# Kernel optimization log

Hardware: AMD Instinct MI355X
Metric: run time of the kernel (lower is better)

The kernel has to match this reference:

```python
import jax, jax.numpy as jnp
import numpy as np

EMBED, HEADS, LEVELS, POINTS = 256, 8, 4, 4
SPATIAL_SHAPES = np.array([[128, 128], [64, 64], [32, 32], [16, 16]], dtype=np.int32)


def _grid_init_bias():
    # Faithful reproduction of the sampling_offsets bias init (per-head directional grid).
    thetas = np.arange(HEADS, dtype=np.float32) * (2.0 * np.pi / HEADS)
    g = np.stack([np.cos(thetas), np.sin(thetas)], -1)
    g = g / np.abs(g).max(-1, keepdims=True)
    g = np.tile(g.reshape(HEADS, 1, 1, 2), (1, LEVELS, POINTS, 1))
    for i in range(POINTS):
        g[:, :, i, :] *= i + 1
    return g.reshape(-1).astype(np.float32)


def setup_inputs() -> dict:
    key = jax.random.key(0)
    ks = jax.random.split(key, 8)
    bs = 2
    V = int((SPATIAL_SHAPES[:, 0] * SPATIAL_SHAPES[:, 1]).sum())  # 21760
    Q = V  # encoder self-attention
    C = EMBED
    n_off = HEADS * LEVELS * POINTS * 2
    n_attn = HEADS * LEVELS * POINTS
    inv_sqrt_c = 1.0 / np.sqrt(C)
    return {
        "query": jax.random.normal(ks[0], (bs, Q, C), jnp.float32),
        "value": jax.random.normal(ks[1], (bs, V, C), jnp.float32),
        "reference_points": jax.random.uniform(ks[2], (bs, Q, LEVELS, 2), jnp.float32),
        "spatial_shapes": SPATIAL_SHAPES,  # static int array
        # learned parameters (torch Linear stored as [in, out]: y = x @ W + b)
        "W_off": jax.random.normal(ks[3], (C, n_off), jnp.float32) * 0.01,
        "b_off": jnp.asarray(_grid_init_bias()),
        "W_attn": jax.random.normal(ks[4], (C, n_attn), jnp.float32) * 0.02,
        "b_attn": jnp.zeros((n_attn,), jnp.float32),
        "W_v": jax.random.normal(ks[5], (C, C), jnp.float32) * inv_sqrt_c,
        "b_v": jnp.zeros((C,), jnp.float32),
        "W_out": jax.random.normal(ks[6], (C, C), jnp.float32) * inv_sqrt_c,
        "b_out": jnp.zeros((C,), jnp.float32),
    }


def _ms_deform_attn(query, value, reference_points, shapes,
                    W_off, b_off, W_attn, b_attn, W_v, b_v, W_out, b_out):
    bs, Q, C = query.shape
    d = C // HEADS
    # value projection -> [bs, heads, V, d]
    val = (value @ W_v + b_v).reshape(bs, -1, HEADS, d).transpose(0, 2, 1, 3)
    # sampling offsets and attention weights from query
    off = (query @ W_off + b_off).reshape(bs, Q, HEADS, LEVELS, POINTS, 2)
    attn = jax.nn.softmax(
        (query @ W_attn + b_attn).reshape(bs, Q, HEADS, LEVELS * POINTS), axis=-1
    ).reshape(bs, Q, HEADS, LEVELS, POINTS)
    # offset normalizer is (W, H) per level
    norm = jnp.asarray(np.stack([shapes[:, 1], shapes[:, 0]], -1), jnp.float32)  # [L,2]
    loc = reference_points[:, :, None, :, None, :] + off / norm[None, None, None, :, None, :]

    out = jnp.zeros((bs, HEADS, Q, d), query.dtype)
    start = 0
    for l in range(LEVELS):
        H, W = int(shapes[l, 0]), int(shapes[l, 1])
        v_l = val[:, :, start:start + H * W]  # [bs, heads, H*W, d]
        start += H * W
        loc_l = loc[:, :, :, l]    # [bs, Q, heads, P, 2] in [0,1]
        attn_l = attn[:, :, :, l]  # [bs, Q, heads, P]
        # grid_sample(align_corners=False, padding_mode='zeros') semantics
        g = 2.0 * loc_l - 1.0
        x = (g[..., 0] + 1.0) * 0.5 * W - 0.5
        y = (g[..., 1] + 1.0) * 0.5 * H - 0.5
        x0 = jnp.floor(x)
        y0 = jnp.floor(y)
        for dx in (0, 1):
            for dy in (0, 1):
                xi = x0 + dx
                yi = y0 + dy
                w = (1.0 - jnp.abs(x - xi)) * (1.0 - jnp.abs(y - yi))
                valid = (xi >= 0) & (xi <= W - 1) & (yi >= 0) & (yi <= H - 1)
                w = jnp.where(valid, w, 0.0) * attn_l  # fused corner + attention weight
                idx = (jnp.clip(yi, 0, H - 1).astype(jnp.int32) * W
                       + jnp.clip(xi, 0, W - 1).astype(jnp.int32))  # [bs,Q,heads,P]
                idx_t = jnp.transpose(idx, (0, 2, 1, 3)).reshape(bs, HEADS, Q * POINTS)
                vals = jnp.take_along_axis(v_l, idx_t[..., None], axis=2)
                vals = vals.reshape(bs, HEADS, Q, POINTS, d)
                out = out + jnp.einsum('bhqpd,bqhp->bhqd', vals, w)
    out = out.transpose(0, 2, 1, 3).reshape(bs, Q, C)  # heads-major channel layout
    return out @ W_out + b_out


def reference(query, value, reference_points, spatial_shapes,
              W_off, b_off, W_attn, b_attn, W_v, b_v, W_out, b_out):
    shapes = np.asarray(spatial_shapes)  # static
    return _ms_deform_attn(query, value, reference_points, shapes,
                           W_off, b_off, W_attn, b_attn, W_v, b_v, W_out, b_out)
```

## Files before the change

kernel.cpp:

```cpp
#include <hip/hip_runtime.h>
#include <math.h>

#define EMBED 256
#define HEADS 8
#define LEVELS 4
#define POINTS 4
#define QN 21760
#define BS 2
#define MTOT (BS * QN)

typedef __attribute__((ext_vector_type(8))) short bf16x8;
typedef __attribute__((ext_vector_type(4))) float f32x4;
typedef __attribute__((ext_vector_type(2))) float f32x2;

__device__ inline ushort f2bf(float f) {
  union { float f; uint u; } v; v.f = f;
  uint r = (v.u + 0x7FFFu + ((v.u >> 16) & 1u)) >> 16;
  return (ushort)r;
}
__device__ inline float bflo(uint u) { union { uint u; float f; } v; v.u = u << 16; return v.f; }
__device__ inline float bfhi(uint u) { union { uint u; float f; } v; v.u = u & 0xFFFF0000u; return v.f; }
__device__ inline uint pk2(float lo, float hi) { return (uint)f2bf(lo) | ((uint)f2bf(hi) << 16); }

__device__ inline void g2l(const ushort* g, ushort* l) {
  __builtin_amdgcn_global_load_lds(
      (const __attribute__((address_space(1))) void*)g,
      (__attribute__((address_space(3))) void*)l, 16, 0, 0);
}

__global__ __launch_bounds__(256) void cast_bf16(const float* __restrict__ x,
                                                 ushort* __restrict__ y) {
  int i = blockIdx.x * 256 + threadIdx.x;
  const float4* xp = (const float4*)x;
  float4 a = xp[2 * i], b = xp[2 * i + 1];
  uint4 o;
  o.x = pk2(a.x, a.y); o.y = pk2(a.z, a.w);
  o.z = pk2(b.x, b.y); o.w = pk2(b.z, b.w);
  ((uint4*)y)[i] = o;
}

__global__ __launch_bounds__(256) void prep_w(const float* __restrict__ W,
                                              ushort* __restrict__ Wt, int N) {
  int idx = blockIdx.x * 256 + threadIdx.x;
  int n = idx >> 8, k = idx & 255;
  Wt[idx] = f2bf(W[(size_t)k * N + n]);
}

__global__ __launch_bounds__(256) void prep_wofflog(
    const float* __restrict__ Woff, const float* __restrict__ Wattn,
    const float* __restrict__ boff, const float* __restrict__ battn,
    ushort* __restrict__ Wt, float* __restrict__ biasf) {
  int idx = blockIdx.x * 256 + threadIdx.x;
  int n = idx >> 8, k = idx & 255;
  float v = (n < 256) ? Woff[(size_t)k * 256 + n] : Wattn[(size_t)k * 128 + (n - 256)];
  Wt[idx] = f2bf(v);
  if (idx < 384) biasf[idx] = (idx < 256) ? boff[idx] : battn[idx - 256];
}

template<int MODE>
__global__ __launch_bounds__(256) void gemm_bf16(
    const ushort* __restrict__ A, const ushort* __restrict__ Bt,
    const float* __restrict__ bias, void* __restrict__ Cout, int N) {
  __shared__ ushort As[128 * 32];
  __shared__ ushort Bs[128 * 32];
  const int t = threadIdx.x, wave = t >> 6, lane = t & 63;
  const int bm = blockIdx.y * 128, bn = blockIdx.x * 128;
  const int wm = (wave >> 1) * 64, wn = (wave & 1) * 64;
  const int l15 = lane & 15, l4 = lane >> 4;

  const int srow = lane >> 2, sch = lane & 3;
  const ushort* Ag = A + (size_t)(bm + 32 * wave + srow) * 256 + sch * 8;
  const ushort* Bg = Bt + (size_t)(bn + 32 * wave + srow) * 256 + sch * 8;
  ushort* la = &As[(32 * wave) * 32];
  ushort* lb = &Bs[(32 * wave) * 32];

  f32x4 acc[4][4];
#pragma unroll
  for (int i = 0; i < 4; ++i)
#pragma unroll
    for (int j = 0; j < 4; ++j) acc[i][j] = (f32x4){0.f, 0.f, 0.f, 0.f};

  for (int k0 = 0; k0 < 256; k0 += 32) {
    __syncthreads();
    g2l(Ag + k0, la);
    g2l(Ag + 16 * 256 + k0, la + 16 * 32);
    g2l(Bg + k0, lb);
    g2l(Bg + 16 * 256 + k0, lb + 16 * 32);
    __syncthreads();

    bf16x8 af[4], bfr[4];
#pragma unroll
    for (int mi = 0; mi < 4; ++mi) af[mi] = *(const bf16x8*)&As[(wm + mi * 16 + l15) * 32 + l4 * 8];
#pragma unroll
    for (int ni = 0; ni < 4; ++ni) bfr[ni] = *(const bf16x8*)&Bs[(wn + ni * 16 + l15) * 32 + l4 * 8];
#pragma unroll
    for (int mi = 0; mi < 4; ++mi)
#pragma unroll
      for (int ni = 0; ni < 4; ++ni)
        acc[mi][ni] = __builtin_amdgcn_mfma_f32_16x16x32_bf16(af[mi], bfr[ni], acc[mi][ni], 0, 0, 0);
  }

#pragma unroll
  for (int mi = 0; mi < 4; ++mi) {
#pragma unroll
    for (int ni = 0; ni < 4; ++ni) {
      int col = bn + wn + ni * 16 + l15;
      float bv = bias[col];
#pragma unroll
      for (int r = 0; r < 4; ++r) {
        int row = bm + wm + mi * 16 + l4 * 4 + r;
        float v = acc[mi][ni][r] + bv;
        if (MODE == 0) {
          ((float*)Cout)[(size_t)row * N + col] = v;
        } else {
          int b = (row >= QN) ? 1 : 0;
          int vpos = row - b * QN;
          int h = col >> 5, c = col & 31;
          ((ushort*)Cout)[((size_t)(b * 8 + h) * QN + vpos) * 32 + c] = f2bf(v);
        }
      }
    }
  }
}

__global__ __launch_bounds__(256) void msda_sample(
    const ushort* __restrict__ val, const float* __restrict__ offlog,
    const float* __restrict__ ref, ushort* __restrict__ interm) {
  const int lsz[LEVELS]    = {128, 64, 32, 16};
  const int lstart[LEVELS] = {0, 16384, 20480, 21504};

  int h   = blockIdx.x & 7;
  int z   = blockIdx.x >> 3;
  int sub = threadIdx.x & 3;
  int bq  = z * 64 + (threadIdx.x >> 2);
  int b   = (bq >= QN) ? 1 : 0;

  const float* lg = offlog + (size_t)bq * 384 + 256 + h * 16;
  float w[16];
  float m = -1e30f;
#pragma unroll
  for (int s = 0; s < 16; ++s) { w[s] = lg[s]; m = fmaxf(m, w[s]); }
  float sum = 0.f;
#pragma unroll
  for (int s = 0; s < 16; ++s) { w[s] = __expf(w[s] - m); sum += w[s]; }
  float inv = 1.f / sum;

  const float* offp = offlog + (size_t)bq * 384 + h * 32;
  const float* refp = ref + (size_t)bq * 8;
  const ushort* vb  = val + ((size_t)(b * 8 + h) * QN) * 32 + sub * 8;

  f32x2 a0 = {0.f, 0.f}, a1 = {0.f, 0.f}, a2 = {0.f, 0.f}, a3 = {0.f, 0.f};

#pragma unroll
  for (int l = 0; l < LEVELS; ++l) {
    const int   W = lsz[l];
    const float fW = (float)W;
    const int   base = lstart[l];
    const float rx = refp[l * 2 + 0], ry = refp[l * 2 + 1];
#pragma unroll
    for (int p = 0; p < POINTS; ++p) {
      float ox = offp[(l * 4 + p) * 2 + 0];
      float oy = offp[(l * 4 + p) * 2 + 1];
      float x = rx * fW + ox - 0.5f;
      float y = ry * fW + oy - 0.5f;
      float x0f = floorf(x), y0f = floorf(y);
      int   x0 = (int)x0f,   y0 = (int)y0f;
      float fx = x - x0f,    fy = y - y0f;
      float a = w[l * 4 + p] * inv;
      int x0c = min(max(x0, 0), W - 1);
      int x1c = min(max(x0 + 1, 0), W - 1);
      int y0c = min(max(y0, 0), W - 1);
      int y1c = min(max(y0 + 1, 0), W - 1);
      float wx0 = (x0 >= 0 && x0 < W) ? (1.f - fx) : 0.f;
      float wx1 = (x0 + 1 >= 0 && x0 + 1 < W) ? fx : 0.f;
      float wy0 = (y0 >= 0 && y0 < W) ? (1.f - fy) : 0.f;
      float wy1 = (y0 + 1 >= 0 && y0 + 1 < W) ? fy : 0.f;
      float w00 = wx0 * wy0 * a, w10 = wx1 * wy0 * a;
      float w01 = wx0 * wy1 * a, w11 = wx1 * wy1 * a;

      const uint4* p00 = (const uint4*)(vb + (size_t)(base + y0c * W + x0c) * 32);
      const uint4* p10 = (const uint4*)(vb + (size_t)(base + y0c * W + x1c) * 32);
      const uint4* p01 = (const uint4*)(vb + (size_t)(base + y1c * W + x0c) * 32);
      const uint4* p11 = (const uint4*)(vb + (size_t)(base + y1c * W + x1c) * 32);
      uint4 u00 = *p00;
      uint4 u10 = *p10;
      uint4 u01 = *p01;
      uint4 u11 = *p11;

      {
        f32x2 wv = {w00, w00}; f32x2 v;
        v.x = bflo(u00.x); v.y = bfhi(u00.x); a0 += v * wv;
        v.x = bflo(u00.y); v.y = bfhi(u00.y); a1 += v * wv;
        v.x = bflo(u00.z); v.y = bfhi(u00.z); a2 += v * wv;
        v.x = bflo(u00.w); v.y = bfhi(u00.w); a3 += v * wv;
      }
      {
        f32x2 wv = {w10, w10}; f32x2 v;
        v.x = bflo(u10.x); v.y = bfhi(u10.x); a0 += v * wv;
        v.x = bflo(u10.y); v.y = bfhi(u10.y); a1 += v * wv;
        v.x = bflo(u10.z); v.y = bfhi(u10.z); a2 += v * wv;
        v.x = bflo(u10.w); v.y = bfhi(u10.w); a3 += v * wv;
      }
      {
        f32x2 wv = {w01, w01}; f32x2 v;
        v.x = bflo(u01.x); v.y = bfhi(u01.x); a0 += v * wv;
        v.x = bflo(u01.y); v.y = bfhi(u01.y); a1 += v * wv;
        v.x = bflo(u01.z); v.y = bfhi(u01.z); a2 += v * wv;
        v.x = bflo(u01.w); v.y = bfhi(u01.w); a3 += v * wv;
      }
      {
        f32x2 wv = {w11, w11}; f32x2 v;
        v.x = bflo(u11.x); v.y = bfhi(u11.x); a0 += v * wv;
        v.x = bflo(u11.y); v.y = bfhi(u11.y); a1 += v * wv;
        v.x = bflo(u11.z); v.y = bfhi(u11.z); a2 += v * wv;
        v.x = bflo(u11.w); v.y = bfhi(u11.w); a3 += v * wv;
      }
    }
  }

  uint4 o;
  o.x = pk2(a0.x, a0.y); o.y = pk2(a1.x, a1.y);
  o.z = pk2(a2.x, a2.y); o.w = pk2(a3.x, a3.y);
  *(uint4*)(interm + (size_t)bq * 256 + h * 32 + sub * 8) = o;
}

extern "C" void kernel_launch(void* const* d_in, const int* in_sizes, int n_in,
                              void* d_out, int out_size, void* d_ws, size_t ws_size,
                              hipStream_t stream) {
  const float* query = (const float*)d_in[0];
  const float* value = (const float*)d_in[1];
  const float* ref   = (const float*)d_in[2];
  const float* W_off  = (const float*)d_in[4];
  const float* b_off  = (const float*)d_in[5];
  const float* W_attn = (const float*)d_in[6];
  const float* b_attn = (const float*)d_in[7];
  const float* W_v    = (const float*)d_in[8];
  const float* b_v    = (const float*)d_in[9];
  const float* W_out  = (const float*)d_in[10];
  const float* b_out  = (const float*)d_in[11];
  float* out = (float*)d_out;

  const size_t szBQC = (size_t)MTOT * EMBED;

  char* wsb = (char*)d_ws;
  ushort* ws_wv      = (ushort*)(wsb + 0);
  ushort* ws_wofflog = (ushort*)(wsb + 131072);
  ushort* ws_wout    = (ushort*)(wsb + 327680);
  float*  ws_biasf   = (float*)(wsb + 458752);
  ushort* ws_val     = (ushort*)(wsb + 462848);
  ushort* ws_q       = (ushort*)(wsb + 22745088);
  ushort* ws_interm  = ws_q;
  ushort* ws_v       = (ushort*)(wsb + 45027328);
  float*  ws_offlog  = (float*)(wsb + 45027328);
  size_t need = 45027328 + 66846720;
  if (ws_size < need) return;

  dim3 blk(256);

  prep_w<<<dim3(256), blk, 0, stream>>>(W_v, ws_wv, 256);
  prep_w<<<dim3(256), blk, 0, stream>>>(W_out, ws_wout, 256);
  prep_wofflog<<<dim3(384), blk, 0, stream>>>(W_off, W_attn, b_off, b_attn, ws_wofflog, ws_biasf);

  cast_bf16<<<dim3(szBQC / 8 / 256), blk, 0, stream>>>(query, ws_q);
  cast_bf16<<<dim3(szBQC / 8 / 256), blk, 0, stream>>>(value, ws_v);

  gemm_bf16<1><<<dim3(2, MTOT / 128), blk, 0, stream>>>(ws_v, ws_wv, b_v, ws_val, 256);
  gemm_bf16<0><<<dim3(3, MTOT / 128), blk, 0, stream>>>(ws_q, ws_wofflog, ws_biasf, ws_offlog, 384);
  msda_sample<<<dim3(680 * 8), blk, 0, stream>>>(ws_val, ws_offlog, ref, ws_interm);
  gemm_bf16<0><<<dim3(2, MTOT / 128), blk, 0, stream>>>(ws_interm, ws_wout, b_out, out, 256);
}
```

Baseline: 314.2 us.

## Fuse casts into input GEMMs, double-buffer GEMMs, and widen sampling per thread

The fp32→bf16 casts of query and value are folded into a single combined input GEMM that converts on the fly while staging tiles into LDS, removing two cast kernels and their round trips through memory. The three weight-prep launches are merged into one. Both GEMMs now double-buffer LDS so the next k-slice loads while MFMAs run. The sampler uses 2 threads per query-head with 16 channels each, vectorized offset and logit loads, and skips corner loads whose weight is zero. That skip drops the index clamping, relying on zero weight to guard out-of-range corners.

New measurement: 303.7 us. 3.4% less time.

```diff
diff --git a/kernel.cpp b/kernel.cpp
--- a/kernel.cpp
+++ b/kernel.cpp
@@ -1,13 +1,8 @@
 #include <hip/hip_runtime.h>
 #include <math.h>
 
-#define EMBED 256
-#define HEADS 8
-#define LEVELS 4
-#define POINTS 4
 #define QN 21760
-#define BS 2
-#define MTOT (BS * QN)
+#define MTOT 43520
 
 typedef __attribute__((ext_vector_type(8))) short bf16x8;
 typedef __attribute__((ext_vector_type(4))) float f32x4;
@@ -15,8 +10,7 @@
 
 __device__ inline ushort f2bf(float f) {
   union { float f; uint u; } v; v.f = f;
-  uint r = (v.u + 0x7FFFu + ((v.u >> 16) & 1u)) >> 16;
-  return (ushort)r;
+  return (ushort)((v.u + 0x7FFFu + ((v.u >> 16) & 1u)) >> 16);
 }
 __device__ inline float bflo(uint u) { union { uint u; float f; } v; v.u = u << 16; return v.f; }
 __device__ inline float bfhi(uint u) { union { uint u; float f; } v; v.u = u & 0xFFFF0000u; return v.f; }
@@ -28,41 +22,139 @@
       (__attribute__((address_space(3))) void*)l, 16, 0, 0);
 }
 
-__global__ __launch_bounds__(256) void cast_bf16(const float* __restrict__ x,
-                                                 ushort* __restrict__ y) {
-  int i = blockIdx.x * 256 + threadIdx.x;
-  const float4* xp = (const float4*)x;
-  float4 a = xp[2 * i], b = xp[2 * i + 1];
-  uint4 o;
-  o.x = pk2(a.x, a.y); o.y = pk2(a.z, a.w);
-  o.z = pk2(b.x, b.y); o.w = pk2(b.z, b.w);
-  ((uint4*)y)[i] = o;
-}
-
-__global__ __launch_bounds__(256) void prep_w(const float* __restrict__ W,
-                                              ushort* __restrict__ Wt, int N) {
-  int idx = blockIdx.x * 256 + threadIdx.x;
-  int n = idx >> 8, k = idx & 255;
-  Wt[idx] = f2bf(W[(size_t)k * N + n]);
-}
-
-__global__ __launch_bounds__(256) void prep_wofflog(
+__global__ __launch_bounds__(256) void prep_weights(
+    const float* __restrict__ Wv, const float* __restrict__ Wout,
     const float* __restrict__ Woff, const float* __restrict__ Wattn,
     const float* __restrict__ boff, const float* __restrict__ battn,
-    ushort* __restrict__ Wt, float* __restrict__ biasf) {
-  int idx = blockIdx.x * 256 + threadIdx.x;
-  int n = idx >> 8, k = idx & 255;
-  float v = (n < 256) ? Woff[(size_t)k * 256 + n] : Wattn[(size_t)k * 128 + (n - 256)];
-  Wt[idx] = f2bf(v);
-  if (idx < 384) biasf[idx] = (idx < 256) ? boff[idx] : battn[idx - 256];
-}
-
-template<int MODE>
-__global__ __launch_bounds__(256) void gemm_bf16(
+    ushort* __restrict__ wv_t, ushort* __restrict__ wout_t,
+    ushort* __restrict__ wol_t, float* __restrict__ biasf) {
+  int bidx = blockIdx.x, t = threadIdx.x;
+  if (bidx < 256) {
+    int idx = bidx * 256 + t; int n = idx >> 8, k = idx & 255;
+    wv_t[idx] = f2bf(Wv[(size_t)k * 256 + n]);
+  } else if (bidx < 512) {
+    int idx = (bidx - 256) * 256 + t; int n = idx >> 8, k = idx & 255;
+    wout_t[idx] = f2bf(Wout[(size_t)k * 256 + n]);
+  } else {
+    int idx = (bidx - 512) * 256 + t; int n = idx >> 8, k = idx & 255;
+    float v = (n < 256) ? Woff[(size_t)k * 256 + n] : Wattn[(size_t)k * 128 + (n - 256)];
+    wol_t[idx] = f2bf(v);
+    if (idx < 384) biasf[idx] = (idx < 256) ? boff[idx] : battn[idx - 256];
+  }
+}
+
+__global__ __launch_bounds__(256) void gemm_in(
+    const float* __restrict__ value, const float* __restrict__ query,
+    const ushort* __restrict__ Wv, const ushort* __restrict__ Wol,
+    const float* __restrict__ bv, const float* __restrict__ bol,
+    ushort* __restrict__ val_out, float* __restrict__ offlog) {
+  __shared__ ushort As[2][4096];
+  __shared__ ushort Bs[2][4096];
+  const int t = threadIdx.x, wave = t >> 6, lane = t & 63;
+  const int bx = blockIdx.x, bm = blockIdx.y * 128;
+  const bool isVal = bx < 2;
+  const float* A = isVal ? value : query;
+  const ushort* Bt = isVal ? (Wv + (size_t)bx * 128 * 256)
+                           : (Wol + (size_t)(bx - 2) * 128 * 256);
+  const int wm = (wave >> 1) * 64, wn = (wave & 1) * 64;
+  const int l15 = lane & 15, l4 = lane >> 4;
+
+  const int srow = lane >> 2, sch = lane & 3;
+  const ushort* Bg = Bt + (size_t)(32 * wave + srow) * 256 + sch * 8;
+  ushort* lb[2] = { &Bs[0][(32 * wave) * 32], &Bs[1][(32 * wave) * 32] };
+
+  f32x4 acc[4][4];
+#pragma unroll
+  for (int i = 0; i < 4; ++i)
+#pragma unroll
+    for (int j = 0; j < 4; ++j) acc[i][j] = (f32x4){0.f, 0.f, 0.f, 0.f};
+
+  {
+    float4 pa[4];
+#pragma unroll
+    for (int i = 0; i < 4; ++i) {
+      int c = t + i * 256; int row = c >> 3, part = c & 7;
+      pa[i] = *(const float4*)&A[(size_t)(bm + row) * 256 + part * 4];
+    }
+    g2l(Bg, lb[0]); g2l(Bg + 16 * 256, lb[0] + 16 * 32);
+#pragma unroll
+    for (int i = 0; i < 4; ++i) {
+      int c = t + i * 256; int row = c >> 3, part = c & 7;
+      ushort4 hv = { f2bf(pa[i].x), f2bf(pa[i].y), f2bf(pa[i].z), f2bf(pa[i].w) };
+      *(ushort4*)&As[0][row * 32 + part * 4] = hv;
+    }
+  }
+
+  for (int k = 0; k < 8; ++k) {
+    __syncthreads();
+    const int cur = k & 1, nxt = cur ^ 1;
+    float4 pa[4];
+    if (k < 7) {
+      int k1 = (k + 1) * 32;
+#pragma unroll
+      for (int i = 0; i < 4; ++i) {
+        int c = t + i * 256; int row = c >> 3, part = c & 7;
+        pa[i] = *(const float4*)&A[(size_t)(bm + row) * 256 + k1 + part * 4];
+      }
+      g2l(Bg + k1, lb[nxt]); g2l(Bg + 16 * 256 + k1, lb[nxt] + 16 * 32);
+    }
+    bf16x8 af[4], bfr[4];
+#pragma unroll
+    for (int mi = 0; mi < 4; ++mi) af[mi] = *(const bf16x8*)&As[cur][(wm + mi * 16 + l15) * 32 + l4 * 8];
+#pragma unroll
+    for (int ni = 0; ni < 4; ++ni) bfr[ni] = *(const bf16x8*)&Bs[cur][(wn + ni * 16 + l15) * 32 + l4 * 8];
+#pragma unroll
+    for (int mi = 0; mi < 4; ++mi)
+#pragma unroll
+      for (int ni = 0; ni < 4; ++ni)
+        acc[mi][ni] = __builtin_amdgcn_mfma_f32_16x16x32_bf16(af[mi], bfr[ni], acc[mi][ni], 0, 0, 0);
+    if (k < 7) {
+#pragma unroll
+      for (int i = 0; i < 4; ++i) {
+        int c = t + i * 256; int row = c >> 3, part = c & 7;
+        ushort4 hv = { f2bf(pa[i].x), f2bf(pa[i].y), f2bf(pa[i].z), f2bf(pa[i].w) };
+        *(ushort4*)&As[nxt][row * 32 + part * 4] = hv;
+      }
+    }
+  }
+
+  if (isVal) {
+#pragma unroll
+    for (int mi = 0; mi < 4; ++mi)
+#pragma unroll
+      for (int ni = 0; ni < 4; ++ni) {
+        int col = bx * 128 + wn + ni * 16 + l15;
+        float bb = bv[col];
+        int hh = col >> 5, c = col & 31;
+#pragma unroll
+        for (int r = 0; r < 4; ++r) {
+          int row = bm + wm + mi * 16 + l4 * 4 + r;
+          int b = (row >= QN) ? 1 : 0;
+          int vpos = row - b * QN;
+          val_out[((size_t)(b * 8 + hh) * QN + vpos) * 32 + c] = f2bf(acc[mi][ni][r] + bb);
+        }
+      }
+  } else {
+#pragma unroll
+    for (int mi = 0; mi < 4; ++mi)
+#pragma unroll
+      for (int ni = 0; ni < 4; ++ni) {
+        int col = (bx - 2) * 128 + wn + ni * 16 + l15;
+        float bb = bol[col];
+#pragma unroll
+        for (int r = 0; r < 4; ++r) {
+          int row = bm + wm + mi * 16 + l4 * 4 + r;
+          offlog[(size_t)row * 384 + col] = acc[mi][ni][r] + bb;
+        }
+      }
+  }
+}
+
+__global__ __launch_bounds__(256) void gemm_out(
     const ushort* __restrict__ A, const ushort* __restrict__ Bt,
-    const float* __restrict__ bias, void* __restrict__ Cout, int N) {
-  __shared__ ushort As[128 * 32];
-  __shared__ ushort Bs[128 * 32];
+    const float* __restrict__ bias, float* __restrict__ C) {
+  __shared__ ushort As[2][4096];
+  __shared__ ushort Bs[2][4096];
   const int t = threadIdx.x, wave = t >> 6, lane = t & 63;
   const int bm = blockIdx.y * 128, bn = blockIdx.x * 128;
   const int wm = (wave >> 1) * 64, wn = (wave & 1) * 64;
@@ -71,8 +163,8 @@
   const int srow = lane >> 2, sch = lane & 3;
   const ushort* Ag = A + (size_t)(bm + 32 * wave + srow) * 256 + sch * 8;
   const ushort* Bg = Bt + (size_t)(bn + 32 * wave + srow) * 256 + sch * 8;
-  ushort* la = &As[(32 * wave) * 32];
-  ushort* lb = &Bs[(32 * wave) * 32];
+  ushort* la[2] = { &As[0][(32 * wave) * 32], &As[1][(32 * wave) * 32] };
+  ushort* lb[2] = { &Bs[0][(32 * wave) * 32], &Bs[1][(32 * wave) * 32] };
 
   f32x4 acc[4][4];
 #pragma unroll
@@ -80,19 +172,22 @@
 #pragma unroll
     for (int j = 0; j < 4; ++j) acc[i][j] = (f32x4){0.f, 0.f, 0.f, 0.f};
 
-  for (int k0 = 0; k0 < 256; k0 += 32) {
+  g2l(Ag, la[0]); g2l(Ag + 16 * 256, la[0] + 16 * 32);
+  g2l(Bg, lb[0]); g2l(Bg + 16 * 256, lb[0] + 16 * 32);
+
+  for (int k = 0; k < 8; ++k) {
     __syncthreads();
-    g2l(Ag + k0, la);
-    g2l(Ag + 16 * 256 + k0, la + 16 * 32);
-    g2l(Bg + k0, lb);
-    g2l(Bg + 16 * 256 + k0, lb + 16 * 32);
-    __syncthreads();
-
+    const int cur = k & 1, nxt = cur ^ 1;
+    if (k < 7) {
+      int k1 = (k + 1) * 32;
+      g2l(Ag + k1, la[nxt]); g2l(Ag + 16 * 256 + k1, la[nxt] + 16 * 32);
+      g2l(Bg + k1, lb[nxt]); g2l(Bg + 16 * 256 + k1, lb[nxt] + 16 * 32);
+    }
     bf16x8 af[4], bfr[4];
 #pragma unroll
-    for (int mi = 0; mi < 4; ++mi) af[mi] = *(const bf16x8*)&As[(wm + mi * 16 + l15) * 32 + l4 * 8];
-#pragma unroll
-    for (int ni = 0; ni < 4; ++ni) bfr[ni] = *(const bf16x8*)&Bs[(wn + ni * 16 + l15) * 32 + l4 * 8];
+    for (int mi = 0; mi < 4; ++mi) af[mi] = *(const bf16x8*)&As[cur][(wm + mi * 16 + l15) * 32 + l4 * 8];
+#pragma unroll
+    for (int ni = 0; ni < 4; ++ni) bfr[ni] = *(const bf16x8*)&Bs[cur][(wn + ni * 16 + l15) * 32 + l4 * 8];
 #pragma unroll
     for (int mi = 0; mi < 4; ++mi)
 #pragma unroll
@@ -101,45 +196,54 @@
   }
 
 #pragma unroll
-  for (int mi = 0; mi < 4; ++mi) {
+  for (int mi = 0; mi < 4; ++mi)
 #pragma unroll
     for (int ni = 0; ni < 4; ++ni) {
       int col = bn + wn + ni * 16 + l15;
-      float bv = bias[col];
+      float bb = bias[col];
 #pragma unroll
       for (int r = 0; r < 4; ++r) {
         int row = bm + wm + mi * 16 + l4 * 4 + r;
-        float v = acc[mi][ni][r] + bv;
-        if (MODE == 0) {
-          ((float*)Cout)[(size_t)row * N + col] = v;
-        } else {
-          int b = (row >= QN) ? 1 : 0;
-          int vpos = row - b * QN;
-          int h = col >> 5, c = col & 31;
-          ((ushort*)Cout)[((size_t)(b * 8 + h) * QN + vpos) * 32 + c] = f2bf(v);
-        }
-      }
-    }
-  }
+        C[(size_t)row * 256 + col] = acc[mi][ni][r] + bb;
+      }
+    }
+}
+
+__device__ inline void fma8(f32x2* a, uint4 u, float wv) {
+  f32x2 ww = { wv, wv }; f32x2 v;
+  v.x = bflo(u.x); v.y = bfhi(u.x); a[0] += v * ww;
+  v.x = bflo(u.y); v.y = bfhi(u.y); a[1] += v * ww;
+  v.x = bflo(u.z); v.y = bfhi(u.z); a[2] += v * ww;
+  v.x = bflo(u.w); v.y = bfhi(u.w); a[3] += v * ww;
 }
 
 __global__ __launch_bounds__(256) void msda_sample(
     const ushort* __restrict__ val, const float* __restrict__ offlog,
     const float* __restrict__ ref, ushort* __restrict__ interm) {
-  const int lsz[LEVELS]    = {128, 64, 32, 16};
-  const int lstart[LEVELS] = {0, 16384, 20480, 21504};
+  const int lsz[4]    = {128, 64, 32, 16};
+  const int lstart[4] = {0, 16384, 20480, 21504};
 
   int h   = blockIdx.x & 7;
   int z   = blockIdx.x >> 3;
-  int sub = threadIdx.x & 3;
-  int bq  = z * 64 + (threadIdx.x >> 2);
+  int sub = threadIdx.x & 1;
+  int bq  = z * 128 + (threadIdx.x >> 1);
   int b   = (bq >= QN) ? 1 : 0;
 
-  const float* lg = offlog + (size_t)bq * 384 + 256 + h * 16;
+  const float* lgp = offlog + (size_t)bq * 384 + 256 + h * 16;
   float w[16];
+  {
+    float4 a0 = *(const float4*)(lgp);
+    float4 a1 = *(const float4*)(lgp + 4);
+    float4 a2 = *(const float4*)(lgp + 8);
+    float4 a3 = *(const float4*)(lgp + 12);
+    w[0]=a0.x; w[1]=a0.y; w[2]=a0.z; w[3]=a0.w;
+    w[4]=a1.x; w[5]=a1.y; w[6]=a1.z; w[7]=a1.w;
+    w[8]=a2.x; w[9]=a2.y; w[10]=a2.z; w[11]=a2.w;
+    w[12]=a3.x; w[13]=a3.y; w[14]=a3.z; w[15]=a3.w;
+  }
   float m = -1e30f;
 #pragma unroll
-  for (int s = 0; s < 16; ++s) { w[s] = lg[s]; m = fmaxf(m, w[s]); }
+  for (int s = 0; s < 16; ++s) m = fmaxf(m, w[s]);
   float sum = 0.f;
 #pragma unroll
   for (int s = 0; s < 16; ++s) { w[s] = __expf(w[s] - m); sum += w[s]; }
@@ -147,30 +251,30 @@
 
   const float* offp = offlog + (size_t)bq * 384 + h * 32;
   const float* refp = ref + (size_t)bq * 8;
-  const ushort* vb  = val + ((size_t)(b * 8 + h) * QN) * 32 + sub * 8;
-
-  f32x2 a0 = {0.f, 0.f}, a1 = {0.f, 0.f}, a2 = {0.f, 0.f}, a3 = {0.f, 0.f};
-
-#pragma unroll
-  for (int l = 0; l < LEVELS; ++l) {
+  const ushort* vb  = val + ((size_t)(b * 8 + h) * QN) * 32 + sub * 16;
+
+  f32x2 acc[8];
+#pragma unroll
+  for (int i = 0; i < 8; ++i) acc[i] = (f32x2){0.f, 0.f};
+
+#pragma unroll
+  for (int l = 0; l < 4; ++l) {
+    float4 o0 = *(const float4*)(offp + l * 8);
+    float4 o1 = *(const float4*)(offp + l * 8 + 4);
+    float ox[4] = { o0.x, o0.z, o1.x, o1.z };
+    float oy[4] = { o0.y, o0.w, o1.y, o1.w };
     const int   W = lsz[l];
     const float fW = (float)W;
     const int   base = lstart[l];
     const float rx = refp[l * 2 + 0], ry = refp[l * 2 + 1];
 #pragma unroll
-    for (int p = 0; p < POINTS; ++p) {
-      float ox = offp[(l * 4 + p) * 2 + 0];
-      float oy = offp[(l * 4 + p) * 2 + 1];
-      float x = rx * fW + ox - 0.5f;
-      float y = ry * fW + oy - 0.5f;
+    for (int p = 0; p < 4; ++p) {
+      float x = rx * fW + ox[p] - 0.5f;
+      float y = ry * fW + oy[p] - 0.5f;
       float x0f = floorf(x), y0f = floorf(y);
       int   x0 = (int)x0f,   y0 = (int)y0f;
       float fx = x - x0f,    fy = y - y0f;
       float a = w[l * 4 + p] * inv;
-      int x0c = min(max(x0, 0), W - 1);
-      int x1c = min(max(x0 + 1, 0), W - 1);
-      int y0c = min(max(y0, 0), W - 1);
-      int y1c = min(max(y0 + 1, 0), W - 1);
       float wx0 = (x0 >= 0 && x0 < W) ? (1.f - fx) : 0.f;
       float wx1 = (x0 + 1 >= 0 && x0 + 1 < W) ? fx : 0.f;
       float wy0 = (y0 >= 0 && y0 < W) ? (1.f - fy) : 0.f;
@@ -178,50 +282,37 @@
       float w00 = wx0 * wy0 * a, w10 = wx1 * wy0 * a;
       float w01 = wx0 * wy1 * a, w11 = wx1 * wy1 * a;
 
-      const uint4* p00 = (const uint4*)(vb + (size_t)(base + y0c * W + x0c) * 32);
-      const uint4* p10 = (const uint4*)(vb + (size_t)(base + y0c * W + x1c) * 32);
-      const uint4* p01 = (const uint4*)(vb + (size_t)(base + y1c * W + x0c) * 32);
-      const uint4* p11 = (const uint4*)(vb + (size_t)(base + y1c * W + x1c) * 32);
-      uint4 u00 = *p00;
-      uint4 u10 = *p10;
-      uint4 u01 = *p01;
-      uint4 u11 = *p11;
-
-      {
-        f32x2 wv = {w00, w00}; f32x2 v;
-        v.x = bflo(u00.x); v.y = bfhi(u00.x); a0 += v * wv;
-        v.x = bflo(u00.y); v.y = bfhi(u00.y); a1 += v * wv;
-        v.x = bflo(u00.z); v.y = bfhi(u00.z); a2 += v * wv;
-        v.x = bflo(u00.w); v.y = bfhi(u00.w); a3 += v * wv;
-      }
-      {
-        f32x2 wv = {w10, w10}; f32x2 v;
-        v.x = bflo(u10.x); v.y = bfhi(u10.x); a0 += v * wv;
-        v.x = bflo(u10.y); v.y = bfhi(u10.y); a1 += v * wv;
-        v.x = bflo(u10.z); v.y = bfhi(u10.z); a2 += v * wv;
-        v.x = bflo(u10.w); v.y = bfhi(u10.w); a3 += v * wv;
-      }
-      {
-        f32x2 wv = {w01, w01}; f32x2 v;
-        v.x = bflo(u01.x); v.y = bfhi(u01.x); a0 += v * wv;
-        v.x = bflo(u01.y); v.y = bfhi(u01.y); a1 += v * wv;
-        v.x = bflo(u01.z); v.y = bfhi(u01.z); a2 += v * wv;
-        v.x = bflo(u01.w); v.y = bfhi(u01.w); a3 += v * wv;
-      }
-      {
-        f32x2 wv = {w11, w11}; f32x2 v;
-        v.x = bflo(u11.x); v.y = bfhi(u11.x); a0 += v * wv;
-        v.x = bflo(u11.y); v.y = bfhi(u11.y); a1 += v * wv;
-        v.x = bflo(u11.z); v.y = bfhi(u11.z); a2 += v * wv;
-        v.x = bflo(u11.w); v.y = bfhi(u11.w); a3 += v * wv;
-      }
-    }
-  }
-
-  uint4 o;
-  o.x = pk2(a0.x, a0.y); o.y = pk2(a1.x, a1.y);
-  o.z = pk2(a2.x, a2.y); o.w = pk2(a3.x, a3.y);
-  *(uint4*)(interm + (size_t)bq * 256 + h * 32 + sub * 8) = o;
+      if (w00 != 0.f) {
+        const ushort* pp = vb + (size_t)(base + y0 * W + x0) * 32;
+        uint4 u0 = *(const uint4*)pp, u1 = *(const uint4*)(pp + 8);
+        fma8(acc, u0, w00); fma8(acc + 4, u1, w00);
+      }
+      if (w10 != 0.f) {
+        const ushort* pp = vb + (size_t)(base + y0 * W + x0 + 1) * 32;
+        uint4 u0 = *(const uint4*)pp, u1 = *(const uint4*)(pp + 8);
+        fma8(acc, u0, w10); fma8(acc + 4, u1, w10);
+      }
+      if (w01 != 0.f) {
+        const ushort* pp = vb + (size_t)(base + (y0 + 1) * W + x0) * 32;
+        uint4 u0 = *(const uint4*)pp, u1 = *(const uint4*)(pp + 8);
+        fma8(acc, u0, w01); fma8(acc + 4, u1, w01);
+      }
+      if (w11 != 0.f) {
+        const ushort* pp = vb + (size_t)(base + (y0 + 1) * W + x0 + 1) * 32;
+        uint4 u0 = *(const uint4*)pp, u1 = *(const uint4*)(pp + 8);
+        fma8(acc, u0, w11); fma8(acc + 4, u1, w11);
+      }
+    }
+  }
+
+  uint4 q0, q1;
+  q0.x = pk2(acc[0].x, acc[0].y); q0.y = pk2(acc[1].x, acc[1].y);
+  q0.z = pk2(acc[2].x, acc[2].y); q0.w = pk2(acc[3].x, acc[3].y);
+  q1.x = pk2(acc[4].x, acc[4].y); q1.y = pk2(acc[5].x, acc[5].y);
+  q1.z = pk2(acc[6].x, acc[6].y); q1.w = pk2(acc[7].x, acc[7].y);
+  ushort* ip = interm + (size_t)bq * 256 + h * 32 + sub * 16;
+  *(uint4*)ip = q0;
+  *(uint4*)(ip + 8) = q1;
 }
 
 extern "C" void kernel_launch(void* const* d_in, const int* in_sizes, int n_in,
@@ -240,32 +331,22 @@
   const float* b_out  = (const float*)d_in[11];
   float* out = (float*)d_out;
 
-  const size_t szBQC = (size_t)MTOT * EMBED;
-
   char* wsb = (char*)d_ws;
-  ushort* ws_wv      = (ushort*)(wsb + 0);
-  ushort* ws_wofflog = (ushort*)(wsb + 131072);
-  ushort* ws_wout    = (ushort*)(wsb + 327680);
-  float*  ws_biasf   = (float*)(wsb + 458752);
-  ushort* ws_val     = (ushort*)(wsb + 462848);
-  ushort* ws_q       = (ushort*)(wsb + 22745088);
-  ushort* ws_interm  = ws_q;
-  ushort* ws_v       = (ushort*)(wsb + 45027328);
-  float*  ws_offlog  = (float*)(wsb + 45027328);
+  ushort* ws_wv     = (ushort*)(wsb + 0);
+  ushort* ws_wol    = (ushort*)(wsb + 131072);
+  ushort* ws_wout   = (ushort*)(wsb + 327680);
+  float*  ws_biasf  = (float*)(wsb + 458752);
+  ushort* ws_val    = (ushort*)(wsb + 462848);
+  ushort* ws_interm = (ushort*)(wsb + 22745088);
+  float*  ws_offlog = (float*)(wsb + 45027328);
   size_t need = 45027328 + 66846720;
   if (ws_size < need) return;
 
   dim3 blk(256);
-
-  prep_w<<<dim3(256), blk, 0, stream>>>(W_v, ws_wv, 256);
-  prep_w<<<dim3(256), blk, 0, stream>>>(W_out, ws_wout, 256);
-  prep_wofflog<<<dim3(384), blk, 0, stream>>>(W_off, W_attn, b_off, b_attn, ws_wofflog, ws_biasf);
-
-  cast_bf16<<<dim3(szBQC / 8 / 256), blk, 0, stream>>>(query, ws_q);
-  cast_bf16<<<dim3(szBQC / 8 / 256), blk, 0, stream>>>(value, ws_v);
-
-  gemm_bf16<1><<<dim3(2, MTOT / 128), blk, 0, stream>>>(ws_v, ws_wv, b_v, ws_val, 256);
-  gemm_bf16<0><<<dim3(3, MTOT / 128), blk, 0, stream>>>(ws_q, ws_wofflog, ws_biasf, ws_offlog, 384);
-  msda_sample<<<dim3(680 * 8), blk, 0, stream>>>(ws_val, ws_offlog, ref, ws_interm);
-  gemm_bf16<0><<<dim3(2, MTOT / 128), blk, 0, stream>>>(ws_interm, ws_wout, b_out, out, 256);
-}
+  prep_weights<<<dim3(896), blk, 0, stream>>>(W_v, W_out, W_off, W_attn, b_off, b_attn,
+                                              ws_wv, ws_wout, ws_wol, ws_biasf);
+  gemm_in<<<dim3(5, 340), blk, 0, stream>>>(value, query, ws_wv, ws_wol, b_v, ws_biasf,
+                                            ws_val, ws_offlog);
+  msda_sample<<<dim3(2720), blk, 0, stream>>>(ws_val, ws_offlog, ref, ws_interm);
+  gemm_out<<<dim3(2, 340), blk, 0, stream>>>(ws_interm, ws_wout, b_out, out);
+}
```
